# Performance work log

Measured on AMD Instinct MI355X. Metric: run time of the kernel, lower is better.

The kernel has to match this reference:

```python
import jax, jax.numpy as jnp
import numpy as np

B, S, E = 4096, 200, 128
ATT_H, MLP_H = 128, 256


def _glorot(key, shape):
    fan_in, fan_out = shape[0], shape[1]
    lim = np.sqrt(6.0 / (fan_in + fan_out)).astype(np.float32)
    return jax.random.uniform(key, shape, jnp.float32, -lim, lim)


def setup_inputs() -> dict:
    key = jax.random.key(0)
    ks = jax.random.split(key, 10)
    return {
        "behavior_emb": jax.random.normal(ks[0], (B, S, E), jnp.float32),
        "candidate_emb": jax.random.normal(ks[1], (B, E), jnp.float32),
        "fc1_w": _glorot(ks[2], (2 * E, ATT_H)),
        "fc1_b": jnp.zeros((ATT_H,), jnp.float32),
        "fc2_w": _glorot(ks[3], (ATT_H, 1)),
        "fc2_b": jnp.zeros((1,), jnp.float32),
        "mlp1_w": _glorot(ks[4], (2 * E, MLP_H)),
        "mlp1_b": jnp.zeros((MLP_H,), jnp.float32),
        "mlp2_w": _glorot(ks[5], (MLP_H, 1)),
        "mlp2_b": jnp.zeros((1,), jnp.float32),
    }


def reference(behavior_emb, candidate_emb, fc1_w, fc1_b, fc2_w, fc2_b,
              mlp1_w, mlp1_b, mlp2_w, mlp2_b):
    # Attention unit: split fc1 weight so we avoid materializing the concat.
    # concat([beh, cand]) @ fc1_w == beh @ W_b + cand @ W_c
    W_b, W_c = fc1_w[:E], fc1_w[E:]
    h = jax.nn.relu(jnp.einsum('bse,eh->bsh', behavior_emb, W_b)
                    + (candidate_emb @ W_c)[:, None, :] + fc1_b)  # [B,S,H]
    scores = jnp.einsum('bsh,h->bs', h, fc2_w[:, 0]) + fc2_b[0]   # [B,S]
    attn = jax.nn.softmax(scores, axis=-1)                         # [B,S]
    user_interest = jnp.einsum('bse,bs->be', behavior_emb, attn)   # [B,E]
    # MLP head
    x = jnp.concatenate([user_interest, candidate_emb], axis=1)    # [B,2E]
    z = jax.nn.relu(x @ mlp1_w + mlp1_b)
    logit = (z @ mlp2_w + mlp2_b)[:, 0]                            # [B]
    return logit
```

## Files before the change

### kernel.cpp

```cpp
#include <hip/hip_runtime.h>
#include <hip/hip_bf16.h>
#include <stdint.h>

#define BN   4096
#define SN   200
#define EN   128
#define HN   128

typedef __attribute__((ext_vector_type(8)))  short  short8;
typedef __attribute__((ext_vector_type(16))) float  floatx16;

__device__ __forceinline__ unsigned short f2bf(float f) {
  union { float f; uint32_t u; } c; c.f = f;
  uint32_t r = c.u + 0x7fffu + ((c.u >> 16) & 1u);
  return (unsigned short)(r >> 16);
}
__device__ __forceinline__ float bf2f(unsigned short h) {
  union { uint32_t u; float f; } c; c.u = ((uint32_t)h) << 16;
  return c.f;
}
__device__ __forceinline__ float bcast_lane(float v, int l) {
  return __builtin_bit_cast(float, __builtin_amdgcn_readlane(__builtin_bit_cast(int, v), l));
}

__device__ __forceinline__ int aoff(int s, int g) {
  return s * 256 + (((g ^ (s & 15)) << 4));
}

__global__ void din_prep(const float* __restrict__ fc1w, short8* __restrict__ ws_afr) {
  const int t    = blockIdx.x & 7;
  const int wv   = blockIdx.x >> 3;
  const int lane = threadIdx.x;
  const int half = lane >> 5;
  const int hcol = wv * 32 + (lane & 31);
  short8 fr;
  #pragma unroll
  for (int j = 0; j < 8; ++j) {
    int e = t * 16 + half * 8 + j;
    fr[j] = (short)f2bf(fc1w[e * HN + hcol]);
  }
  ws_afr[((wv * 8 + t) << 6) + lane] = fr;
}

__global__ __launch_bounds__(256, 3)
void din_main(const float* __restrict__ behavior, const float* __restrict__ cand,
              const float* __restrict__ fc1w, const float* __restrict__ fc1b,
              const float* __restrict__ fc2w, const short8* __restrict__ ws_afr,
              float* __restrict__ ws_ui) {
  __shared__ unsigned short Abuf[SN * EN];
  __shared__ float scores_s[SN];
  __shared__ float cvec2[2][HN];
  __shared__ float cand_s[EN];
  __shared__ float ui_s[EN];

  const int tid = threadIdx.x;
  const int b   = blockIdx.x;

  if (tid < SN) scores_s[tid] = 0.f;
  if (tid < EN) {
    cand_s[tid] = cand[(size_t)b * EN + tid];
    ui_s[tid]   = 0.f;
  }
  __syncthreads();

  const int wv   = tid >> 6;
  const int lane = tid & 63;
  const int half = lane >> 5;
  const int l31  = lane & 31;

  const float* src = behavior + (size_t)b * SN * EN;
  float4 va[13];
  #pragma unroll
  for (int u = 0; u < 13; ++u) {
    int q = u * 256 + tid;
    va[u] = *(const float4*)(src + (q >> 5) * EN + ((q & 31) << 2));
  }
  short8 afr[8];
  #pragma unroll
  for (int t = 0; t < 8; ++t) afr[t] = ws_afr[((wv * 8 + t) << 6) + lane];

  {
    const int h  = tid & 127;
    const int eh = tid >> 7;
    float p0 = (eh == 0) ? fc1b[h] : 0.f, p1 = 0.f;
    const float* wc = fc1w + (size_t)(EN + eh * 64) * HN + h;
    #pragma unroll 8
    for (int e = 0; e < 64; e += 2) {
      p0 = fmaf(cand_s[eh * 64 + e],     wc[(size_t)e * HN],       p0);
      p1 = fmaf(cand_s[eh * 64 + e + 1], wc[(size_t)(e + 1) * HN], p1);
    }
    cvec2[eh][h] = p0 + p1;
  }

  #pragma unroll
  for (int u = 0; u < 13; ++u) {
    int q = u * 256 + tid, s = q >> 5, e4 = (q & 31) << 2;
    uint32_t p0 = (uint32_t)f2bf(va[u].x) | ((uint32_t)f2bf(va[u].y) << 16);
    uint32_t p1 = (uint32_t)f2bf(va[u].z) | ((uint32_t)f2bf(va[u].w) << 16);
    char* dst = (char*)Abuf + s * 256 + ((((e4 >> 3) ^ (s & 15))) << 4) + ((e4 & 7) << 1);
    *(uint2*)dst = make_uint2(p0, p1);
  }
  float4 vb[12];
  #pragma unroll
  for (int u = 0; u < 12; ++u) {
    int q = (u + 13) * 256 + tid;
    vb[u] = *(const float4*)(src + (q >> 5) * EN + ((q & 31) << 2));
  }
  #pragma unroll
  for (int u = 0; u < 12; ++u) {
    int q = (u + 13) * 256 + tid, s = q >> 5, e4 = (q & 31) << 2;
    uint32_t p0 = (uint32_t)f2bf(vb[u].x) | ((uint32_t)f2bf(vb[u].y) << 16);
    uint32_t p1 = (uint32_t)f2bf(vb[u].z) | ((uint32_t)f2bf(vb[u].w) << 16);
    char* dst = (char*)Abuf + s * 256 + ((((e4 >> 3) ^ (s & 15))) << 4) + ((e4 & 7) << 1);
    *(uint2*)dst = make_uint2(p0, p1);
  }
  __syncthreads();

  float cadd[16], wmul[16];
  #pragma unroll
  for (int r = 0; r < 16; ++r) {
    int hr = wv * 32 + (r & 3) + ((r >> 2) << 3) + (half << 2);
    cadd[r] = cvec2[0][hr] + cvec2[1][hr];
    wmul[r] = fc2w[hr];
  }

  for (int st = 0; st < 7; ++st) {
    floatx16 acc = {0.f,0.f,0.f,0.f,0.f,0.f,0.f,0.f,0.f,0.f,0.f,0.f,0.f,0.f,0.f,0.f};
    const int srow = st * 32 + l31;
    const int sr   = (srow < SN) ? srow : (SN - 1);
    #pragma unroll
    for (int t = 0; t < 8; ++t) {
      int g = 2 * t + half;
      const short8 bfr = *(const short8*)((const char*)Abuf + aoff(sr, g));
      acc = __builtin_amdgcn_mfma_f32_32x32x16_bf16(afr[t], bfr, acc, 0, 0, 0);
    }
    float part = 0.f;
    #pragma unroll
    for (int r = 0; r < 16; ++r) {
      float h = fmaxf(acc[r] + cadd[r], 0.f);
      part = fmaf(h, wmul[r], part);
    }
    part += __shfl_xor(part, 32, 64);
    if (lane < 32 && srow < SN) atomicAdd(&scores_s[srow], part);
  }
  __syncthreads();

  if (wv == 0) {
    float v0[4];
    #pragma unroll
    for (int k = 0; k < 4; ++k) {
      int s = k * 64 + lane;
      v0[k] = (s < SN) ? scores_s[s] : -3.0e38f;
    }
    float m = fmaxf(fmaxf(v0[0], v0[1]), fmaxf(v0[2], v0[3]));
    #pragma unroll
    for (int off = 32; off >= 1; off >>= 1) m = fmaxf(m, __shfl_xor(m, off, 64));
    float e0[4], sum = 0.f;
    #pragma unroll
    for (int k = 0; k < 4; ++k) { e0[k] = __expf(v0[k] - m); sum += e0[k]; }
    #pragma unroll
    for (int off = 32; off >= 1; off >>= 1) sum += __shfl_xor(sum, off, 64);
    float inv = 1.0f / sum;
    #pragma unroll
    for (int k = 0; k < 4; ++k) {
      int s = k * 64 + lane;
      if (s < SN) scores_s[s] = e0[k] * inv;
    }
  }
  __syncthreads();

  {
    const int g  = tid & 15;
    const int sg = tid >> 4;
    float ua[8] = {0.f,0.f,0.f,0.f,0.f,0.f,0.f,0.f};
    for (int s = sg; s < SN; s += 16) {
      float a = scores_s[s];
      const short8 bv = *(const short8*)((const char*)Abuf + aoff(s, g));
      #pragma unroll
      for (int j = 0; j < 8; ++j) ua[j] = fmaf(a, bf2f((unsigned short)bv[j]), ua[j]);
    }
    #pragma unroll
    for (int j = 0; j < 8; ++j) {
      ua[j] += __shfl_xor(ua[j], 16, 64);
      ua[j] += __shfl_xor(ua[j], 32, 64);
    }
    if (lane < 16) {
      #pragma unroll
      for (int j = 0; j < 8; ++j) atomicAdd(&ui_s[(g << 3) + j], ua[j]);
    }
  }
  __syncthreads();
  if (tid < EN) ws_ui[(size_t)b * EN + tid] = ui_s[tid];
}

__global__ __launch_bounds__(256, 4)
void din_mlp(const float* __restrict__ ws_ui, const float* __restrict__ cand,
             const float* __restrict__ w1, const float* __restrict__ b1,
             const float* __restrict__ w2, const float* __restrict__ b2,
             float* __restrict__ out) {
  const int tid  = threadIdx.x;
  const int lane = tid & 63;
  const int wv   = tid >> 6;
  const int r0   = blockIdx.x * 4;

  float xr[4][4];
  #pragma unroll
  for (int r = 0; r < 4; ++r) {
    #pragma unroll
    for (int c = 0; c < 4; ++c) {
      int i = c * 64 + lane;
      int row = r0 + r;
      xr[r][c] = (i < 128) ? ws_ui[row * 128 + i] : cand[row * 128 + (i - 128)];
    }
  }

  const int j = tid;
  const float bj = b1[j];
  float acc[4] = {bj, bj, bj, bj};

  #pragma unroll
  for (int c = 0; c < 4; ++c) {
    #pragma unroll 8
    for (int il = 0; il < 64; ++il) {
      float w = w1[(c * 64 + il) * 256 + j];
      #pragma unroll
      for (int r = 0; r < 4; ++r)
        acc[r] = fmaf(bcast_lane(xr[r][c], il), w, acc[r]);
    }
  }

  const float w2j = w2[j];
  float part[4];
  #pragma unroll
  for (int r = 0; r < 4; ++r) part[r] = fmaxf(acc[r], 0.f) * w2j;
  #pragma unroll
  for (int off = 32; off >= 1; off >>= 1) {
    #pragma unroll
    for (int r = 0; r < 4; ++r) part[r] += __shfl_xor(part[r], off, 64);
  }

  __shared__ float red[4][4];
  if (lane == 0) {
    #pragma unroll
    for (int r = 0; r < 4; ++r) red[wv][r] = part[r];
  }
  __syncthreads();
  if (tid < 4)
    out[r0 + tid] = red[0][tid] + red[1][tid] + red[2][tid] + red[3][tid] + b2[0];
}

extern "C" void kernel_launch(void* const* d_in, const int* in_sizes, int n_in,
                              void* d_out, int out_size, void* d_ws, size_t ws_size,
                              hipStream_t stream) {
  const float* behavior = (const float*)d_in[0];
  const float* cand     = (const float*)d_in[1];
  const float* fc1w     = (const float*)d_in[2];
  const float* fc1b     = (const float*)d_in[3];
  const float* fc2w     = (const float*)d_in[4];
  const float* m1w      = (const float*)d_in[6];
  const float* m1b      = (const float*)d_in[7];
  const float* m2w      = (const float*)d_in[8];
  const float* m2b      = (const float*)d_in[9];
  float* outp  = (float*)d_out;
  float* ws_ui = (float*)d_ws;
  short8* ws_afr = (short8*)((char*)d_ws + (size_t)BN * EN * 4);

  din_prep<<<32, 64, 0, stream>>>(fc1w, ws_afr);
  din_main<<<BN, 256, 0, stream>>>(behavior, cand, fc1w, fc1b, fc2w, ws_afr, ws_ui);
  din_mlp<<<BN / 4, 256, 0, stream>>>(ws_ui, cand, m1w, m1b, m2w, m2b, outp);
}
```

Before: 620.5 us.

## Process eight batch rows per block with register-prefetched next row

```diff
diff --git a/kernel.cpp b/kernel.cpp
--- a/kernel.cpp
+++ b/kernel.cpp
@@ -6,6 +6,8 @@
 #define SN   200
 #define EN   128
 #define HN   128
+#define ROWS 8
+#define NBLK (BN / ROWS)
 
 typedef __attribute__((ext_vector_type(8)))  short  short8;
 typedef __attribute__((ext_vector_type(16))) float  floatx16;
@@ -18,6 +20,14 @@
 __device__ __forceinline__ float bf2f(unsigned short h) {
   union { uint32_t u; float f; } c; c.u = ((uint32_t)h) << 16;
   return c.f;
+}
+__device__ __forceinline__ uint32_t pk2(float x, float y) {
+#if defined(__has_builtin) && __has_builtin(__builtin_amdgcn_cvt_pk_bf16_f32)
+  typedef __bf16 bf16x2 __attribute__((ext_vector_type(2)));
+  return __builtin_bit_cast(uint32_t, __builtin_amdgcn_cvt_pk_bf16_f32(x, y));
+#else
+  return (uint32_t)f2bf(x) | ((uint32_t)f2bf(y) << 16);
+#endif
 }
 __device__ __forceinline__ float bcast_lane(float v, int l) {
   return __builtin_bit_cast(float, __builtin_amdgcn_readlane(__builtin_bit_cast(int, v), l));
@@ -42,155 +52,218 @@
   ws_afr[((wv * 8 + t) << 6) + lane] = fr;
 }
 
-__global__ __launch_bounds__(256, 3)
+__global__ __launch_bounds__(256, 2)
 void din_main(const float* __restrict__ behavior, const float* __restrict__ cand,
               const float* __restrict__ fc1w, const float* __restrict__ fc1b,
               const float* __restrict__ fc2w, const short8* __restrict__ ws_afr,
               float* __restrict__ ws_ui) {
   __shared__ unsigned short Abuf[SN * EN];
   __shared__ float scores_s[SN];
-  __shared__ float cvec2[2][HN];
-  __shared__ float cand_s[EN];
+  __shared__ float attn_s[SN];
+  __shared__ float cvec_all[2][ROWS][HN];
+  __shared__ float candT[EN][ROWS];
   __shared__ float ui_s[EN];
 
-  const int tid = threadIdx.x;
-  const int b   = blockIdx.x;
-
-  if (tid < SN) scores_s[tid] = 0.f;
-  if (tid < EN) {
-    cand_s[tid] = cand[(size_t)b * EN + tid];
-    ui_s[tid]   = 0.f;
-  }
-  __syncthreads();
-
+  const int tid  = threadIdx.x;
+  const int b    = blockIdx.x;
   const int wv   = tid >> 6;
   const int lane = tid & 63;
   const int half = lane >> 5;
   const int l31  = lane & 31;
 
-  const float* src = behavior + (size_t)b * SN * EN;
-  float4 va[13];
+  if (tid < SN) scores_s[tid] = 0.f;
+  if (tid < EN) ui_s[tid] = 0.f;
+
+  {
+    const float4 v = ((const float4*)(cand + (size_t)b * ROWS * EN))[tid];
+    const int f = tid * 4;
+    #pragma unroll
+    for (int j = 0; j < 4; ++j) candT[(f + j) & 127][(f + j) >> 7] = v[j];
+  }
+
+  const float* src0 = behavior + (size_t)b * ROWS * SN * EN;
+  float4 va[13], vb[12];
   #pragma unroll
   for (int u = 0; u < 13; ++u) {
     int q = u * 256 + tid;
-    va[u] = *(const float4*)(src + (q >> 5) * EN + ((q & 31) << 2));
-  }
+    va[u] = *(const float4*)(src0 + (q >> 5) * EN + ((q & 31) << 2));
+  }
+  #pragma unroll
+  for (int u = 0; u < 12; ++u) {
+    int q = (u + 13) * 256 + tid;
+    vb[u] = *(const float4*)(src0 + (q >> 5) * EN + ((q & 31) << 2));
+  }
+
   short8 afr[8];
   #pragma unroll
   for (int t = 0; t < 8; ++t) afr[t] = ws_afr[((wv * 8 + t) << 6) + lane];
+  float wmul[16];
+  #pragma unroll
+  for (int i = 0; i < 16; ++i)
+    wmul[i] = fc2w[wv * 32 + (i & 3) + ((i >> 2) << 3) + (half << 2)];
+
+  __syncthreads();
 
   {
     const int h  = tid & 127;
     const int eh = tid >> 7;
-    float p0 = (eh == 0) ? fc1b[h] : 0.f, p1 = 0.f;
+    float p[ROWS];
+    const float pb = (eh == 0) ? fc1b[h] : 0.f;
+    #pragma unroll
+    for (int r = 0; r < ROWS; ++r) p[r] = (r == 0) ? pb : 0.f;
+    if (eh == 0) {
+      #pragma unroll
+      for (int r = 1; r < ROWS; ++r) p[r] = pb;
+      p[0] = pb;
+    }
     const float* wc = fc1w + (size_t)(EN + eh * 64) * HN + h;
     #pragma unroll 8
-    for (int e = 0; e < 64; e += 2) {
-      p0 = fmaf(cand_s[eh * 64 + e],     wc[(size_t)e * HN],       p0);
-      p1 = fmaf(cand_s[eh * 64 + e + 1], wc[(size_t)(e + 1) * HN], p1);
-    }
-    cvec2[eh][h] = p0 + p1;
+    for (int e = 0; e < 64; ++e) {
+      float w = wc[(size_t)e * HN];
+      const float4* cp = (const float4*)&candT[eh * 64 + e][0];
+      float4 c0 = cp[0], c1 = cp[1];
+      p[0] = fmaf(c0.x, w, p[0]); p[1] = fmaf(c0.y, w, p[1]);
+      p[2] = fmaf(c0.z, w, p[2]); p[3] = fmaf(c0.w, w, p[3]);
+      p[4] = fmaf(c1.x, w, p[4]); p[5] = fmaf(c1.y, w, p[5]);
+      p[6] = fmaf(c1.z, w, p[6]); p[7] = fmaf(c1.w, w, p[7]);
+    }
+    #pragma unroll
+    for (int r = 0; r < ROWS; ++r) cvec_all[eh][r][h] = p[r];
+  }
+  __syncthreads();
+  {
+    float4* d = (float4*)&cvec_all[0][0][0];
+    const float4* s2 = (const float4*)&cvec_all[1][0][0];
+    float4 x = d[tid], y = s2[tid];
+    x.x += y.x; x.y += y.y; x.z += y.z; x.w += y.w;
+    d[tid] = x;
   }
 
   #pragma unroll
   for (int u = 0; u < 13; ++u) {
     int q = u * 256 + tid, s = q >> 5, e4 = (q & 31) << 2;
-    uint32_t p0 = (uint32_t)f2bf(va[u].x) | ((uint32_t)f2bf(va[u].y) << 16);
-    uint32_t p1 = (uint32_t)f2bf(va[u].z) | ((uint32_t)f2bf(va[u].w) << 16);
-    char* dst = (char*)Abuf + s * 256 + ((((e4 >> 3) ^ (s & 15))) << 4) + ((e4 & 7) << 1);
-    *(uint2*)dst = make_uint2(p0, p1);
-  }
-  float4 vb[12];
-  #pragma unroll
-  for (int u = 0; u < 12; ++u) {
-    int q = (u + 13) * 256 + tid;
-    vb[u] = *(const float4*)(src + (q >> 5) * EN + ((q & 31) << 2));
+    uint2 pk = make_uint2(pk2(va[u].x, va[u].y), pk2(va[u].z, va[u].w));
+    *(uint2*)((char*)Abuf + s * 256 + ((((e4 >> 3) ^ (s & 15))) << 4) + ((e4 & 7) << 1)) = pk;
   }
   #pragma unroll
   for (int u = 0; u < 12; ++u) {
     int q = (u + 13) * 256 + tid, s = q >> 5, e4 = (q & 31) << 2;
-    uint32_t p0 = (uint32_t)f2bf(vb[u].x) | ((uint32_t)f2bf(vb[u].y) << 16);
-    uint32_t p1 = (uint32_t)f2bf(vb[u].z) | ((uint32_t)f2bf(vb[u].w) << 16);
-    char* dst = (char*)Abuf + s * 256 + ((((e4 >> 3) ^ (s & 15))) << 4) + ((e4 & 7) << 1);
-    *(uint2*)dst = make_uint2(p0, p1);
+    uint2 pk = make_uint2(pk2(vb[u].x, vb[u].y), pk2(vb[u].z, vb[u].w));
+    *(uint2*)((char*)Abuf + s * 256 + ((((e4 >> 3) ^ (s & 15))) << 4) + ((e4 & 7) << 1)) = pk;
   }
   __syncthreads();
 
-  float cadd[16], wmul[16];
-  #pragma unroll
-  for (int r = 0; r < 16; ++r) {
-    int hr = wv * 32 + (r & 3) + ((r >> 2) << 3) + (half << 2);
-    cadd[r] = cvec2[0][hr] + cvec2[1][hr];
-    wmul[r] = fc2w[hr];
-  }
-
-  for (int st = 0; st < 7; ++st) {
-    floatx16 acc = {0.f,0.f,0.f,0.f,0.f,0.f,0.f,0.f,0.f,0.f,0.f,0.f,0.f,0.f,0.f,0.f};
-    const int srow = st * 32 + l31;
-    const int sr   = (srow < SN) ? srow : (SN - 1);
-    #pragma unroll
-    for (int t = 0; t < 8; ++t) {
-      int g = 2 * t + half;
-      const short8 bfr = *(const short8*)((const char*)Abuf + aoff(sr, g));
-      acc = __builtin_amdgcn_mfma_f32_32x32x16_bf16(afr[t], bfr, acc, 0, 0, 0);
-    }
-    float part = 0.f;
-    #pragma unroll
-    for (int r = 0; r < 16; ++r) {
-      float h = fmaxf(acc[r] + cadd[r], 0.f);
-      part = fmaf(h, wmul[r], part);
-    }
-    part += __shfl_xor(part, 32, 64);
-    if (lane < 32 && srow < SN) atomicAdd(&scores_s[srow], part);
-  }
-  __syncthreads();
-
-  if (wv == 0) {
-    float v0[4];
-    #pragma unroll
-    for (int k = 0; k < 4; ++k) {
-      int s = k * 64 + lane;
-      v0[k] = (s < SN) ? scores_s[s] : -3.0e38f;
-    }
-    float m = fmaxf(fmaxf(v0[0], v0[1]), fmaxf(v0[2], v0[3]));
-    #pragma unroll
-    for (int off = 32; off >= 1; off >>= 1) m = fmaxf(m, __shfl_xor(m, off, 64));
-    float e0[4], sum = 0.f;
-    #pragma unroll
-    for (int k = 0; k < 4; ++k) { e0[k] = __expf(v0[k] - m); sum += e0[k]; }
-    #pragma unroll
-    for (int off = 32; off >= 1; off >>= 1) sum += __shfl_xor(sum, off, 64);
-    float inv = 1.0f / sum;
-    #pragma unroll
-    for (int k = 0; k < 4; ++k) {
-      int s = k * 64 + lane;
-      if (s < SN) scores_s[s] = e0[k] * inv;
-    }
-  }
-  __syncthreads();
-
-  {
-    const int g  = tid & 15;
-    const int sg = tid >> 4;
-    float ua[8] = {0.f,0.f,0.f,0.f,0.f,0.f,0.f,0.f};
-    for (int s = sg; s < SN; s += 16) {
-      float a = scores_s[s];
-      const short8 bv = *(const short8*)((const char*)Abuf + aoff(s, g));
-      #pragma unroll
-      for (int j = 0; j < 8; ++j) ua[j] = fmaf(a, bf2f((unsigned short)bv[j]), ua[j]);
-    }
-    #pragma unroll
-    for (int j = 0; j < 8; ++j) {
-      ua[j] += __shfl_xor(ua[j], 16, 64);
-      ua[j] += __shfl_xor(ua[j], 32, 64);
-    }
-    if (lane < 16) {
-      #pragma unroll
-      for (int j = 0; j < 8; ++j) atomicAdd(&ui_s[(g << 3) + j], ua[j]);
-    }
-  }
-  __syncthreads();
-  if (tid < EN) ws_ui[(size_t)b * EN + tid] = ui_s[tid];
+  for (int r = 0; r < ROWS; ++r) {
+    const int row = b * ROWS + r;
+    const float* srcn = src0 + (size_t)(r + 1) * SN * EN;
+
+    if (r < ROWS - 1) {
+      #pragma unroll
+      for (int u = 0; u < 13; ++u) {
+        int q = u * 256 + tid;
+        va[u] = *(const float4*)(srcn + (q >> 5) * EN + ((q & 31) << 2));
+      }
+    }
+
+    float cadd[16];
+    #pragma unroll
+    for (int i = 0; i < 16; ++i)
+      cadd[i] = cvec_all[0][r][wv * 32 + (i & 3) + ((i >> 2) << 3) + (half << 2)];
+
+    for (int st = 0; st < 7; ++st) {
+      floatx16 acc;
+      #pragma unroll
+      for (int i = 0; i < 16; ++i) acc[i] = cadd[i];
+      const int srow = st * 32 + l31;
+      const int sr   = (srow < SN) ? srow : (SN - 1);
+      #pragma unroll
+      for (int t = 0; t < 8; ++t) {
+        const short8 bfr = *(const short8*)((const char*)Abuf + aoff(sr, 2 * t + half));
+        acc = __builtin_amdgcn_mfma_f32_32x32x16_bf16(afr[t], bfr, acc, 0, 0, 0);
+      }
+      float part = 0.f;
+      #pragma unroll
+      for (int i = 0; i < 16; ++i)
+        part = fmaf(fmaxf(acc[i], 0.f), wmul[i], part);
+      part += __shfl_xor(part, 32, 64);
+      if (lane < 32 && srow < SN) atomicAdd(&scores_s[srow], part);
+    }
+
+    if (r < ROWS - 1) {
+      #pragma unroll
+      for (int u = 0; u < 12; ++u) {
+        int q = (u + 13) * 256 + tid;
+        vb[u] = *(const float4*)(srcn + (q >> 5) * EN + ((q & 31) << 2));
+      }
+    }
+    __syncthreads();
+
+    if (wv == 0) {
+      float v0[4];
+      #pragma unroll
+      for (int k = 0; k < 4; ++k) {
+        int s = k * 64 + lane;
+        v0[k] = (s < SN) ? scores_s[s] : -3.0e38f;
+      }
+      float m = fmaxf(fmaxf(v0[0], v0[1]), fmaxf(v0[2], v0[3]));
+      #pragma unroll
+      for (int off = 32; off >= 1; off >>= 1) m = fmaxf(m, __shfl_xor(m, off, 64));
+      float e0[4], sum = 0.f;
+      #pragma unroll
+      for (int k = 0; k < 4; ++k) { e0[k] = __expf(v0[k] - m); sum += e0[k]; }
+      #pragma unroll
+      for (int off = 32; off >= 1; off >>= 1) sum += __shfl_xor(sum, off, 64);
+      float inv = 1.0f / sum;
+      #pragma unroll
+      for (int k = 0; k < 4; ++k) {
+        int s = k * 64 + lane;
+        if (s < SN) { attn_s[s] = e0[k] * inv; scores_s[s] = 0.f; }
+      }
+    }
+    __syncthreads();
+
+    {
+      const int g  = tid & 15;
+      const int sg = tid >> 4;
+      float ua[8] = {0.f,0.f,0.f,0.f,0.f,0.f,0.f,0.f};
+      for (int s = sg; s < SN; s += 16) {
+        float a = attn_s[s];
+        const short8 bv = *(const short8*)((const char*)Abuf + aoff(s, g));
+        #pragma unroll
+        for (int j = 0; j < 8; ++j) ua[j] = fmaf(a, bf2f((unsigned short)bv[j]), ua[j]);
+      }
+      #pragma unroll
+      for (int j = 0; j < 8; ++j) {
+        ua[j] += __shfl_xor(ua[j], 16, 64);
+        ua[j] += __shfl_xor(ua[j], 32, 64);
+      }
+      if (lane < 16) {
+        #pragma unroll
+        for (int j = 0; j < 8; ++j) atomicAdd(&ui_s[(g << 3) + j], ua[j]);
+      }
+    }
+    __syncthreads();
+
+    if (tid < EN) {
+      ws_ui[(size_t)row * EN + tid] = ui_s[tid];
+      ui_s[tid] = 0.f;
+    }
+    if (r < ROWS - 1) {
+      #pragma unroll
+      for (int u = 0; u < 13; ++u) {
+        int q = u * 256 + tid, s = q >> 5, e4 = (q & 31) << 2;
+        uint2 pk = make_uint2(pk2(va[u].x, va[u].y), pk2(va[u].z, va[u].w));
+        *(uint2*)((char*)Abuf + s * 256 + ((((e4 >> 3) ^ (s & 15))) << 4) + ((e4 & 7) << 1)) = pk;
+      }
+      #pragma unroll
+      for (int u = 0; u < 12; ++u) {
+        int q = (u + 13) * 256 + tid, s = q >> 5, e4 = (q & 31) << 2;
+        uint2 pk = make_uint2(pk2(vb[u].x, vb[u].y), pk2(vb[u].z, vb[u].w));
+        *(uint2*)((char*)Abuf + s * 256 + ((((e4 >> 3) ^ (s & 15))) << 4) + ((e4 & 7) << 1)) = pk;
+      }
+    }
+    __syncthreads();
+  }
 }
 
 __global__ __launch_bounds__(256, 4)
@@ -266,6 +339,6 @@
   short8* ws_afr = (short8*)((char*)d_ws + (size_t)BN * EN * 4);
 
   din_prep<<<32, 64, 0, stream>>>(fc1w, ws_afr);
-  din_main<<<BN, 256, 0, stream>>>(behavior, cand, fc1w, fc1b, fc2w, ws_afr, ws_ui);
+  din_main<<<NBLK, 256, 0, stream>>>(behavior, cand, fc1w, fc1b, fc2w, ws_afr, ws_ui);
   din_mlp<<<BN / 4, 256, 0, stream>>>(ws_ui, cand, m1w, m1b, m2w, m2b, outp);
 }
```

After: 810.8 us. +30.7%, slower.

## Fuse attention and MLP into persistent kernel with async LDS row prefetch

Applied to the files above, without the earlier changes.

```diff
diff --git a/kernel.cpp b/kernel.cpp
--- a/kernel.cpp
+++ b/kernel.cpp
@@ -6,6 +6,8 @@
 #define SN   200
 #define EN   128
 #define HN   128
+#define ROWS 16
+#define NBLK (BN / ROWS)
 
 typedef __attribute__((ext_vector_type(8)))  short  short8;
 typedef __attribute__((ext_vector_type(16))) float  floatx16;
@@ -19,12 +21,32 @@
   union { uint32_t u; float f; } c; c.u = ((uint32_t)h) << 16;
   return c.f;
 }
-__device__ __forceinline__ float bcast_lane(float v, int l) {
-  return __builtin_bit_cast(float, __builtin_amdgcn_readlane(__builtin_bit_cast(int, v), l));
+__device__ __forceinline__ uint32_t pk2(float x, float y) {
+#if defined(__has_builtin) && __has_builtin(__builtin_amdgcn_cvt_pk_bf16_f32)
+  typedef __bf16 bf16x2 __attribute__((ext_vector_type(2)));
+  return __builtin_bit_cast(uint32_t, __builtin_amdgcn_cvt_pk_bf16_f32(x, y));
+#else
+  return (uint32_t)f2bf(x) | ((uint32_t)f2bf(y) << 16);
+#endif
 }
 
 __device__ __forceinline__ int aoff(int s, int g) {
   return s * 256 + (((g ^ (s & 15)) << 4));
+}
+
+__device__ __forceinline__ void issue_row(const float* __restrict__ src,
+                                          float* stage, int wv, int lane) {
+  #pragma unroll
+  for (int k = 0; k < 13; ++k) {
+    int c = wv + k * 8;
+    if (c < 100) {
+      const float* g = src + c * 256 + lane * 4;
+      __builtin_amdgcn_global_load_lds(
+          (const __attribute__((address_space(1))) void*)g,
+          (__attribute__((address_space(3))) void*)(stage + c * 256),
+          16, 0, 0);
+    }
+  }
 }
 
 __global__ void din_prep(const float* __restrict__ fc1w, short8* __restrict__ ws_afr) {
@@ -42,211 +64,202 @@
   ws_afr[((wv * 8 + t) << 6) + lane] = fr;
 }
 
-__global__ __launch_bounds__(256, 3)
-void din_main(const float* __restrict__ behavior, const float* __restrict__ cand,
-              const float* __restrict__ fc1w, const float* __restrict__ fc1b,
-              const float* __restrict__ fc2w, const short8* __restrict__ ws_afr,
-              float* __restrict__ ws_ui) {
+__global__ __launch_bounds__(512, 2)
+void din_fused(const float* __restrict__ behavior, const float* __restrict__ cand,
+               const float* __restrict__ fc1w, const float* __restrict__ fc1b,
+               const float* __restrict__ fc2w, const float* __restrict__ m1w,
+               const float* __restrict__ m1b, const float* __restrict__ m2w,
+               const float* __restrict__ m2b, const short8* __restrict__ ws_afr,
+               float* __restrict__ out) {
+  __shared__ float          stage[SN * EN];
   __shared__ unsigned short Abuf[SN * EN];
-  __shared__ float scores_s[SN];
-  __shared__ float cvec2[2][HN];
-  __shared__ float cand_s[EN];
-  __shared__ float ui_s[EN];
-
-  const int tid = threadIdx.x;
-  const int b   = blockIdx.x;
-
-  if (tid < SN) scores_s[tid] = 0.f;
-  if (tid < EN) {
-    cand_s[tid] = cand[(size_t)b * EN + tid];
-    ui_s[tid]   = 0.f;
-  }
-  __syncthreads();
-
+  __shared__ float          cvec2[4][HN];
+  __shared__ float          scores_s[SN];
+  __shared__ float          ui_s[EN];
+  __shared__ float          cand_row[EN];
+  __shared__ float          zpart[256];
+  __shared__ float          red[4];
+
+  const int tid  = threadIdx.x;
+  const int b    = blockIdx.x;
   const int wv   = tid >> 6;
   const int lane = tid & 63;
   const int half = lane >> 5;
   const int l31  = lane & 31;
-
-  const float* src = behavior + (size_t)b * SN * EN;
-  float4 va[13];
-  #pragma unroll
-  for (int u = 0; u < 13; ++u) {
-    int q = u * 256 + tid;
-    va[u] = *(const float4*)(src + (q >> 5) * EN + ((q & 31) << 2));
-  }
+  const int ht   = wv & 3;
+  const float* src0 = behavior + (size_t)b * ROWS * SN * EN;
+
+  issue_row(src0, stage, wv, lane);
+
   short8 afr[8];
   #pragma unroll
-  for (int t = 0; t < 8; ++t) afr[t] = ws_afr[((wv * 8 + t) << 6) + lane];
-
-  {
-    const int h  = tid & 127;
-    const int eh = tid >> 7;
-    float p0 = (eh == 0) ? fc1b[h] : 0.f, p1 = 0.f;
-    const float* wc = fc1w + (size_t)(EN + eh * 64) * HN + h;
-    #pragma unroll 8
-    for (int e = 0; e < 64; e += 2) {
-      p0 = fmaf(cand_s[eh * 64 + e],     wc[(size_t)e * HN],       p0);
-      p1 = fmaf(cand_s[eh * 64 + e + 1], wc[(size_t)(e + 1) * HN], p1);
-    }
-    cvec2[eh][h] = p0 + p1;
-  }
-
-  #pragma unroll
-  for (int u = 0; u < 13; ++u) {
-    int q = u * 256 + tid, s = q >> 5, e4 = (q & 31) << 2;
-    uint32_t p0 = (uint32_t)f2bf(va[u].x) | ((uint32_t)f2bf(va[u].y) << 16);
-    uint32_t p1 = (uint32_t)f2bf(va[u].z) | ((uint32_t)f2bf(va[u].w) << 16);
-    char* dst = (char*)Abuf + s * 256 + ((((e4 >> 3) ^ (s & 15))) << 4) + ((e4 & 7) << 1);
-    *(uint2*)dst = make_uint2(p0, p1);
-  }
-  float4 vb[12];
-  #pragma unroll
-  for (int u = 0; u < 12; ++u) {
-    int q = (u + 13) * 256 + tid;
-    vb[u] = *(const float4*)(src + (q >> 5) * EN + ((q & 31) << 2));
-  }
-  #pragma unroll
-  for (int u = 0; u < 12; ++u) {
-    int q = (u + 13) * 256 + tid, s = q >> 5, e4 = (q & 31) << 2;
-    uint32_t p0 = (uint32_t)f2bf(vb[u].x) | ((uint32_t)f2bf(vb[u].y) << 16);
-    uint32_t p1 = (uint32_t)f2bf(vb[u].z) | ((uint32_t)f2bf(vb[u].w) << 16);
-    char* dst = (char*)Abuf + s * 256 + ((((e4 >> 3) ^ (s & 15))) << 4) + ((e4 & 7) << 1);
-    *(uint2*)dst = make_uint2(p0, p1);
-  }
+  for (int t = 0; t < 8; ++t) afr[t] = ws_afr[((ht * 8 + t) << 6) + lane];
+  float wmul[16];
+  #pragma unroll
+  for (int i = 0; i < 16; ++i)
+    wmul[i] = fc2w[ht * 32 + (i & 3) + ((i >> 2) << 3) + (half << 2)];
+  const int   jj  = tid & 255;
+  const int   ehm = tid >> 8;
+  const float b1j = m1b[jj];
+  const float w2j = m2w[jj];
+  const float b2s = m2b[0];
+  const float fb  = fc1b[tid & 127];
+
+  if (tid < SN) scores_s[tid] = 0.f;
+  if (tid < EN) {
+    ui_s[tid]     = 0.f;
+    cand_row[tid] = cand[(size_t)b * ROWS * EN + tid];
+  }
+
+  asm volatile("s_waitcnt vmcnt(0)" ::: "memory");
+  #pragma unroll
+  for (int it = 0; it < 13; ++it) {
+    int q = it * 512 + tid;
+    if (it < 12 || tid < 256) {
+      float4 v = *(const float4*)&stage[q * 4];
+      int s = q >> 5, e4 = (q & 31) << 2;
+      uint2 pk = make_uint2(pk2(v.x, v.y), pk2(v.z, v.w));
+      *(uint2*)((char*)Abuf + s * 256 + ((((e4 >> 3) ^ (s & 15))) << 4) + ((e4 & 7) << 1)) = pk;
+    }
+  }
+  if (ROWS > 1) issue_row(src0 + (size_t)SN * EN, stage, wv, lane);
   __syncthreads();
 
-  float cadd[16], wmul[16];
-  #pragma unroll
-  for (int r = 0; r < 16; ++r) {
-    int hr = wv * 32 + (r & 3) + ((r >> 2) << 3) + (half << 2);
-    cadd[r] = cvec2[0][hr] + cvec2[1][hr];
-    wmul[r] = fc2w[hr];
-  }
-
-  for (int st = 0; st < 7; ++st) {
-    floatx16 acc = {0.f,0.f,0.f,0.f,0.f,0.f,0.f,0.f,0.f,0.f,0.f,0.f,0.f,0.f,0.f,0.f};
-    const int srow = st * 32 + l31;
-    const int sr   = (srow < SN) ? srow : (SN - 1);
-    #pragma unroll
-    for (int t = 0; t < 8; ++t) {
-      int g = 2 * t + half;
-      const short8 bfr = *(const short8*)((const char*)Abuf + aoff(sr, g));
-      acc = __builtin_amdgcn_mfma_f32_32x32x16_bf16(afr[t], bfr, acc, 0, 0, 0);
-    }
-    float part = 0.f;
-    #pragma unroll
-    for (int r = 0; r < 16; ++r) {
-      float h = fmaxf(acc[r] + cadd[r], 0.f);
-      part = fmaf(h, wmul[r], part);
-    }
-    part += __shfl_xor(part, 32, 64);
-    if (lane < 32 && srow < SN) atomicAdd(&scores_s[srow], part);
-  }
-  __syncthreads();
-
-  if (wv == 0) {
-    float v0[4];
-    #pragma unroll
-    for (int k = 0; k < 4; ++k) {
-      int s = k * 64 + lane;
-      v0[k] = (s < SN) ? scores_s[s] : -3.0e38f;
-    }
-    float m = fmaxf(fmaxf(v0[0], v0[1]), fmaxf(v0[2], v0[3]));
-    #pragma unroll
-    for (int off = 32; off >= 1; off >>= 1) m = fmaxf(m, __shfl_xor(m, off, 64));
-    float e0[4], sum = 0.f;
-    #pragma unroll
-    for (int k = 0; k < 4; ++k) { e0[k] = __expf(v0[k] - m); sum += e0[k]; }
-    #pragma unroll
-    for (int off = 32; off >= 1; off >>= 1) sum += __shfl_xor(sum, off, 64);
-    float inv = 1.0f / sum;
-    #pragma unroll
-    for (int k = 0; k < 4; ++k) {
-      int s = k * 64 + lane;
-      if (s < SN) scores_s[s] = e0[k] * inv;
-    }
-  }
-  __syncthreads();
-
-  {
-    const int g  = tid & 15;
-    const int sg = tid >> 4;
-    float ua[8] = {0.f,0.f,0.f,0.f,0.f,0.f,0.f,0.f};
-    for (int s = sg; s < SN; s += 16) {
-      float a = scores_s[s];
-      const short8 bv = *(const short8*)((const char*)Abuf + aoff(s, g));
-      #pragma unroll
-      for (int j = 0; j < 8; ++j) ua[j] = fmaf(a, bf2f((unsigned short)bv[j]), ua[j]);
-    }
-    #pragma unroll
-    for (int j = 0; j < 8; ++j) {
-      ua[j] += __shfl_xor(ua[j], 16, 64);
-      ua[j] += __shfl_xor(ua[j], 32, 64);
-    }
-    if (lane < 16) {
-      #pragma unroll
-      for (int j = 0; j < 8; ++j) atomicAdd(&ui_s[(g << 3) + j], ua[j]);
-    }
-  }
-  __syncthreads();
-  if (tid < EN) ws_ui[(size_t)b * EN + tid] = ui_s[tid];
-}
-
-__global__ __launch_bounds__(256, 4)
-void din_mlp(const float* __restrict__ ws_ui, const float* __restrict__ cand,
-             const float* __restrict__ w1, const float* __restrict__ b1,
-             const float* __restrict__ w2, const float* __restrict__ b2,
-             float* __restrict__ out) {
-  const int tid  = threadIdx.x;
-  const int lane = tid & 63;
-  const int wv   = tid >> 6;
-  const int r0   = blockIdx.x * 4;
-
-  float xr[4][4];
-  #pragma unroll
-  for (int r = 0; r < 4; ++r) {
-    #pragma unroll
-    for (int c = 0; c < 4; ++c) {
-      int i = c * 64 + lane;
-      int row = r0 + r;
-      xr[r][c] = (i < 128) ? ws_ui[row * 128 + i] : cand[row * 128 + (i - 128)];
-    }
-  }
-
-  const int j = tid;
-  const float bj = b1[j];
-  float acc[4] = {bj, bj, bj, bj};
-
-  #pragma unroll
-  for (int c = 0; c < 4; ++c) {
-    #pragma unroll 8
-    for (int il = 0; il < 64; ++il) {
-      float w = w1[(c * 64 + il) * 256 + j];
-      #pragma unroll
-      for (int r = 0; r < 4; ++r)
-        acc[r] = fmaf(bcast_lane(xr[r][c], il), w, acc[r]);
-    }
-  }
-
-  const float w2j = w2[j];
-  float part[4];
-  #pragma unroll
-  for (int r = 0; r < 4; ++r) part[r] = fmaxf(acc[r], 0.f) * w2j;
-  #pragma unroll
-  for (int off = 32; off >= 1; off >>= 1) {
-    #pragma unroll
-    for (int r = 0; r < 4; ++r) part[r] += __shfl_xor(part[r], off, 64);
-  }
-
-  __shared__ float red[4][4];
-  if (lane == 0) {
-    #pragma unroll
-    for (int r = 0; r < 4; ++r) red[wv][r] = part[r];
-  }
-  __syncthreads();
-  if (tid < 4)
-    out[r0 + tid] = red[0][tid] + red[1][tid] + red[2][tid] + red[3][tid] + b2[0];
+  for (int r = 0; r < ROWS; ++r) {
+    const size_t row = (size_t)b * ROWS + r;
+
+    {
+      const int h = tid & 127, eq = tid >> 7;
+      float p = (eq == 0) ? fb : 0.f;
+      const float* wc = fc1w + (size_t)(EN + eq * 32) * HN + h;
+      #pragma unroll 8
+      for (int e = 0; e < 32; ++e)
+        p = fmaf(cand_row[eq * 32 + e], wc[(size_t)e * HN], p);
+      cvec2[eq][h] = p;
+    }
+    __syncthreads();
+    if (tid < HN)
+      cvec2[0][tid] += cvec2[1][tid] + cvec2[2][tid] + cvec2[3][tid];
+    __syncthreads();
+
+    float cadd[16];
+    {
+      const float4* cb = (const float4*)&cvec2[0][ht * 32 + (half << 2)];
+      #pragma unroll
+      for (int blk = 0; blk < 4; ++blk) {
+        float4 v = cb[blk * 2];
+        cadd[blk * 4 + 0] = v.x; cadd[blk * 4 + 1] = v.y;
+        cadd[blk * 4 + 2] = v.z; cadd[blk * 4 + 3] = v.w;
+      }
+    }
+
+    for (int st = (wv >> 2); st < 7; st += 2) {
+      floatx16 acc;
+      #pragma unroll
+      for (int i = 0; i < 16; ++i) acc[i] = cadd[i];
+      const int srow = st * 32 + l31;
+      const int sr   = (srow < SN) ? srow : (SN - 1);
+      #pragma unroll
+      for (int t = 0; t < 8; ++t) {
+        const short8 bfr = *(const short8*)((const char*)Abuf + aoff(sr, 2 * t + half));
+        acc = __builtin_amdgcn_mfma_f32_32x32x16_bf16(afr[t], bfr, acc, 0, 0, 0);
+      }
+      float part = 0.f;
+      #pragma unroll
+      for (int i = 0; i < 16; ++i)
+        part = fmaf(fmaxf(acc[i], 0.f), wmul[i], part);
+      part += __shfl_xor(part, 32, 64);
+      if (lane < 32 && srow < SN) atomicAdd(&scores_s[srow], part);
+    }
+    __syncthreads();
+
+    if (wv == 0) {
+      float v0[4];
+      #pragma unroll
+      for (int k = 0; k < 4; ++k) {
+        int s = k * 64 + lane;
+        v0[k] = (s < SN) ? scores_s[s] : -3.0e38f;
+      }
+      float m = fmaxf(fmaxf(v0[0], v0[1]), fmaxf(v0[2], v0[3]));
+      #pragma unroll
+      for (int off = 32; off >= 1; off >>= 1) m = fmaxf(m, __shfl_xor(m, off, 64));
+      float e0[4], sum = 0.f;
+      #pragma unroll
+      for (int k = 0; k < 4; ++k) { e0[k] = __expf(v0[k] - m); sum += e0[k]; }
+      #pragma unroll
+      for (int off = 32; off >= 1; off >>= 1) sum += __shfl_xor(sum, off, 64);
+      float inv = 1.0f / sum;
+      #pragma unroll
+      for (int k = 0; k < 4; ++k) {
+        int s = k * 64 + lane;
+        if (s < SN) scores_s[s] = e0[k] * inv;
+      }
+    }
+    __syncthreads();
+
+    {
+      const int g  = tid & 15;
+      const int sg = tid >> 4;
+      float ua[8] = {0.f,0.f,0.f,0.f,0.f,0.f,0.f,0.f};
+      for (int s = sg; s < SN; s += 32) {
+        float a = scores_s[s];
+        const short8 bv = *(const short8*)((const char*)Abuf + aoff(s, g));
+        #pragma unroll
+        for (int j = 0; j < 8; ++j) ua[j] = fmaf(a, bf2f((unsigned short)bv[j]), ua[j]);
+      }
+      #pragma unroll
+      for (int j = 0; j < 8; ++j) {
+        ua[j] += __shfl_xor(ua[j], 16, 64);
+        ua[j] += __shfl_xor(ua[j], 32, 64);
+      }
+      if (lane < 16) {
+        #pragma unroll
+        for (int j = 0; j < 8; ++j) atomicAdd(&ui_s[(g << 3) + j], ua[j]);
+      }
+    }
+    float creg = 0.f;
+    if (r + 1 < ROWS && tid < EN) creg = cand[(row + 1) * EN + tid];
+    __syncthreads();
+
+    {
+      float acc = (ehm == 0) ? b1j : 0.f;
+      const float* wp = m1w + (size_t)(ehm * 128) * 256 + jj;
+      #pragma unroll 8
+      for (int ii = 0; ii < 128; ++ii) {
+        float x = (ehm == 0) ? ui_s[ii] : cand_row[ii];
+        acc = fmaf(x, wp[(size_t)ii * 256], acc);
+      }
+      if (ehm == 1) zpart[jj] = acc;
+      __syncthreads();
+      if (ehm == 0) {
+        float z = fmaxf(acc + zpart[jj], 0.f);
+        float part = z * w2j;
+        #pragma unroll
+        for (int off = 32; off >= 1; off >>= 1) part += __shfl_xor(part, off, 64);
+        if (lane == 0) red[wv] = part;
+      }
+      __syncthreads();
+      if (tid == 0) out[row] = red[0] + red[1] + red[2] + red[3] + b2s;
+    }
+
+    if (r + 1 < ROWS) {
+      asm volatile("s_waitcnt vmcnt(0)" ::: "memory");
+      #pragma unroll
+      for (int it = 0; it < 13; ++it) {
+        int q = it * 512 + tid;
+        if (it < 12 || tid < 256) {
+          float4 v = *(const float4*)&stage[q * 4];
+          int s = q >> 5, e4 = (q & 31) << 2;
+          uint2 pk = make_uint2(pk2(v.x, v.y), pk2(v.z, v.w));
+          *(uint2*)((char*)Abuf + s * 256 + ((((e4 >> 3) ^ (s & 15))) << 4) + ((e4 & 7) << 1)) = pk;
+        }
+      }
+      if (r + 2 < ROWS) issue_row(src0 + (size_t)(r + 2) * SN * EN, stage, wv, lane);
+      if (tid < SN) scores_s[tid] = 0.f;
+      if (tid < EN) { ui_s[tid] = 0.f; cand_row[tid] = creg; }
+    }
+    __syncthreads();
+  }
 }
 
 extern "C" void kernel_launch(void* const* d_in, const int* in_sizes, int n_in,
@@ -261,11 +274,10 @@
   const float* m1b      = (const float*)d_in[7];
   const float* m2w      = (const float*)d_in[8];
   const float* m2b      = (const float*)d_in[9];
-  float* outp  = (float*)d_out;
-  float* ws_ui = (float*)d_ws;
-  short8* ws_afr = (short8*)((char*)d_ws + (size_t)BN * EN * 4);
+  float* outp    = (float*)d_out;
+  short8* ws_afr = (short8*)d_ws;
 
   din_prep<<<32, 64, 0, stream>>>(fc1w, ws_afr);
-  din_main<<<BN, 256, 0, stream>>>(behavior, cand, fc1w, fc1b, fc2w, ws_afr, ws_ui);
-  din_mlp<<<BN / 4, 256, 0, stream>>>(ws_ui, cand, m1w, m1b, m2w, m2b, outp);
-}
+  din_fused<<<NBLK, 512, 0, stream>>>(behavior, cand, fc1w, fc1b, fc2w,
+                                      m1w, m1b, m2w, m2b, ws_afr, outp);
+}
```

Result: slower. 695.0 us (+12.0%).
